# Optimization experiments

Measured on AMD Instinct MI355X. Metric: run time of the kernel, lower is better.

Reference implementation:

```python
import jax, jax.numpy as jnp
import numpy as np

D_MODEL = 1024
N_HEADS = 16
HEAD_DIM = D_MODEL // N_HEADS


def setup_inputs() -> dict:
    key = jax.random.key(0)
    ks = jax.random.split(key, 5)
    x = jax.random.normal(ks[0], (4, 2048, D_MODEL), dtype=jnp.float32)
    s = 1.0 / np.sqrt(D_MODEL)
    W_qkv = jax.random.uniform(ks[1], (D_MODEL, 3 * D_MODEL), minval=-s, maxval=s, dtype=jnp.float32)
    b_qkv = jax.random.uniform(ks[2], (3 * D_MODEL,), minval=-s, maxval=s, dtype=jnp.float32)
    W_out = jax.random.uniform(ks[3], (D_MODEL, D_MODEL), minval=-s, maxval=s, dtype=jnp.float32)
    b_out = jax.random.uniform(ks[4], (D_MODEL,), minval=-s, maxval=s, dtype=jnp.float32)
    return {"x": x, "W_qkv": W_qkv, "b_qkv": b_qkv, "W_out": W_out, "b_out": b_out}


def reference(x, W_qkv, b_qkv, W_out, b_out):
    B, S, _ = x.shape
    qkv = x @ W_qkv + b_qkv                                   # [B,S,3*D]
    qkv = qkv.reshape(B, S, 3, N_HEADS, HEAD_DIM)
    qkv = jnp.transpose(qkv, (2, 0, 3, 1, 4))                 # [3,B,H,S,Dh]
    Q, K, V = qkv[0], qkv[1], qkv[2]
    scores = jnp.einsum('bhqd,bhkd->bhqk', Q, K) / np.sqrt(HEAD_DIM)
    attn = jax.nn.softmax(scores, axis=-1)
    out = jnp.einsum('bhqk,bhkd->bhqd', attn, V)              # [B,H,S,Dh]
    out = jnp.transpose(out, (0, 2, 1, 3)).reshape(B, S, D_MODEL)
    return out @ W_out + b_out
```

## Files before the change

### kernel.cpp

```cpp
#include <hip/hip_runtime.h>
#include <stdint.h>

typedef __attribute__((ext_vector_type(8))) short short8;
typedef __attribute__((ext_vector_type(4))) float f32x4;
typedef __attribute__((ext_vector_type(16))) float f32x16;
typedef __attribute__((ext_vector_type(4))) float float4v;
typedef __attribute__((ext_vector_type(4))) unsigned short ushort4v;
typedef __attribute__((ext_vector_type(2))) unsigned int uint2v;
typedef __attribute__((ext_vector_type(4))) unsigned int uint4v;

#define MFMA16(a,b,c) __builtin_amdgcn_mfma_f32_16x16x32_bf16((a),(b),(c),0,0,0)
#define MFMA32(a,b,c) __builtin_amdgcn_mfma_f32_32x32x16_bf16((a),(b),(c),0,0,0)

typedef const __attribute__((address_space(1))) void gld_src_t;
typedef __attribute__((address_space(3))) void gld_dst_t;
#define GLOAD_LDS16(g, l) __builtin_amdgcn_global_load_lds((gld_src_t*)(g), (gld_dst_t*)(l), 16, 0, 0)

__device__ __forceinline__ unsigned short f2bf(float f) {
  union { float f; unsigned int u; } v; v.f = f;
  unsigned int u = v.u;
  unsigned int r = (u + 0x7fffu + ((u >> 16) & 1u)) >> 16;
  return (unsigned short)r;
}

__device__ __forceinline__ unsigned cvtpk(float a, float b) {
  unsigned r;
  asm("v_cvt_pk_bf16_f32 %0, %1, %2" : "=v"(r) : "v"(a), "v"(b));
  return r;
}

__device__ __forceinline__ float fexp2(float x) {
  return __builtin_amdgcn_exp2f(x);
}

__global__ __launch_bounds__(256) void cvt_f32_bf16(const float* __restrict__ in,
                                                    unsigned short* __restrict__ out) {
  int i = blockIdx.x * 256 + threadIdx.x;
  float4v v = ((const float4v*)in)[i];
  ushort4v o;
  o[0] = f2bf(v[0]); o[1] = f2bf(v[1]); o[2] = f2bf(v[2]); o[3] = f2bf(v[3]);
  ((ushort4v*)out)[i] = o;
}

__global__ __launch_bounds__(256) void cvt_transpose(const float* __restrict__ W,
                                                     unsigned short* __restrict__ WT,
                                                     int K, int N) {
  __shared__ unsigned short lds[64][72];
  int k0 = blockIdx.x * 64, n0 = blockIdx.y * 64;
  int t = threadIdx.x, tr = t >> 4, tc = t & 15;
#pragma unroll
  for (int p = 0; p < 4; ++p) {
    int k = tr + p * 16;
    float4v v = *(const float4v*)&W[(size_t)(k0 + k) * N + n0 + tc * 4];
    lds[tc * 4 + 0][k] = f2bf(v[0]);
    lds[tc * 4 + 1][k] = f2bf(v[1]);
    lds[tc * 4 + 2][k] = f2bf(v[2]);
    lds[tc * 4 + 3][k] = f2bf(v[3]);
  }
  __syncthreads();
#pragma unroll
  for (int p = 0; p < 4; ++p) {
    int n = tr + p * 16;
    ushort4v o;
    o[0] = lds[n][tc * 4 + 0]; o[1] = lds[n][tc * 4 + 1];
    o[2] = lds[n][tc * 4 + 2]; o[3] = lds[n][tc * 4 + 3];
    *(ushort4v*)&WT[(size_t)(n0 + n) * K + k0 + tc * 4] = o;
  }
}

__device__ __forceinline__ void gemm_mainloop_128(const unsigned short* __restrict__ A,
                                                  const unsigned short* __restrict__ BT,
                                                  int K, int row0, int col0,
                                                  unsigned short* Als, unsigned short* Bls,
                                                  f32x4 acc[4][4]) {
  int t = threadIdx.x;
  int w = t >> 6, l = t & 63;
  int lo = l & 15, hi = l >> 4;
  int wr = w >> 1, wc = w & 1;
  int srcC = (l & 3) ^ ((l >> 2) & 3) ^ ((l >> 4) & 3);
  const unsigned short* Ag1 = A + (size_t)(row0 + (t >> 2)) * K + srcC * 8;
  const unsigned short* Ag2 = A + (size_t)(row0 + 64 + (t >> 2)) * K + srcC * 8;
  const unsigned short* Bg1 = BT + (size_t)(col0 + (t >> 2)) * K + srcC * 8;
  const unsigned short* Bg2 = BT + (size_t)(col0 + 64 + (t >> 2)) * K + srcC * 8;
  unsigned short* Ald1 = Als + w * 512;
  unsigned short* Ald2 = Als + 2048 + w * 512;
  unsigned short* Bld1 = Bls + w * 512;
  unsigned short* Bld2 = Bls + 2048 + w * 512;
  int fs = (lo & 3) ^ ((lo >> 2) & 3);
  int aoff[4], boff[4];
#pragma unroll
  for (int m = 0; m < 4; ++m) aoff[m] = (wr * 64 + m * 16 + lo) * 32 + ((hi ^ fs) << 3);
#pragma unroll
  for (int n = 0; n < 4; ++n) boff[n] = (wc * 64 + n * 16 + lo) * 32 + ((hi ^ fs) << 3);

  for (int k0 = 0; k0 < K; k0 += 32) {
    GLOAD_LDS16(Ag1 + k0, Ald1);
    GLOAD_LDS16(Ag2 + k0, Ald2);
    GLOAD_LDS16(Bg1 + k0, Bld1);
    GLOAD_LDS16(Bg2 + k0, Bld2);
    __syncthreads();
    short8 af[4], bf[4];
#pragma unroll
    for (int m = 0; m < 4; ++m) af[m] = *(const short8*)&Als[aoff[m]];
#pragma unroll
    for (int n = 0; n < 4; ++n) bf[n] = *(const short8*)&Bls[boff[n]];
#pragma unroll
    for (int m = 0; m < 4; ++m)
#pragma unroll
      for (int n = 0; n < 4; ++n)
        acc[m][n] = MFMA16(af[m], bf[n], acc[m][n]);
    __syncthreads();
  }
}

__global__ __launch_bounds__(256) void gemm_qkv(const unsigned short* __restrict__ xb,
                                                const unsigned short* __restrict__ WT,
                                                const float* __restrict__ bias,
                                                unsigned short* __restrict__ Q,
                                                unsigned short* __restrict__ Ko,
                                                unsigned short* __restrict__ Vt) {
  __shared__ unsigned short Als[4096], Bls[4096];
  f32x4 zero = {0.f, 0.f, 0.f, 0.f};
  f32x4 acc[4][4];
#pragma unroll
  for (int m = 0; m < 4; ++m)
#pragma unroll
    for (int n = 0; n < 4; ++n) acc[m][n] = zero;
  int row0 = blockIdx.x * 128, col0 = blockIdx.y * 128;
  gemm_mainloop_128(xb, WT, 1024, row0, col0, Als, Bls, acc);

  int t = threadIdx.x, w = t >> 6, l = t & 63, lo = l & 15, hi = l >> 4;
  int wr = w >> 1, wc = w & 1;
#pragma unroll
  for (int m = 0; m < 4; ++m) {
#pragma unroll
    for (int n = 0; n < 4; ++n) {
      int col = col0 + wc * 64 + n * 16 + lo;
      float b = bias[col];
      int which = col >> 10, hd = col & 1023, h = hd >> 6, d = hd & 63;
      int row = row0 + wr * 64 + m * 16 + hi * 4;
      int bb = row >> 11, s = row & 2047;
      if (which == 2) {
        ushort4v o;
#pragma unroll
        for (int r = 0; r < 4; ++r) o[r] = f2bf(acc[m][n][r] + b);
        *(ushort4v*)&Vt[((size_t)(bb * 16 + h) * 64 + d) * 2048 + s] = o;
      } else if (which == 0) {
        size_t base = ((size_t)(bb * 16 + h) * 2048 + s) * 64 + d;
#pragma unroll
        for (int r = 0; r < 4; ++r)
          Q[base + (size_t)r * 64] = f2bf((acc[m][n][r] + b) * 0.18033688011112042f);
      } else {
        size_t base = ((size_t)(bb * 16 + h) * 2048 + s) * 64 + d;
#pragma unroll
        for (int r = 0; r < 4; ++r)
          Ko[base + (size_t)r * 64] = f2bf(acc[m][n][r] + b);
      }
    }
  }
}

__global__ __launch_bounds__(256) void gemm_out(const unsigned short* __restrict__ attn,
                                                const unsigned short* __restrict__ WT,
                                                const float* __restrict__ bias,
                                                float* __restrict__ out) {
  __shared__ unsigned short Als[4096], Bls[4096];
  f32x4 zero = {0.f, 0.f, 0.f, 0.f};
  f32x4 acc[4][4];
#pragma unroll
  for (int m = 0; m < 4; ++m)
#pragma unroll
    for (int n = 0; n < 4; ++n) acc[m][n] = zero;
  int row0 = blockIdx.x * 128, col0 = blockIdx.y * 128;
  gemm_mainloop_128(attn, WT, 1024, row0, col0, Als, Bls, acc);

  int t = threadIdx.x, w = t >> 6, l = t & 63, lo = l & 15, hi = l >> 4;
  int wr = w >> 1, wc = w & 1;
#pragma unroll
  for (int m = 0; m < 4; ++m) {
#pragma unroll
    for (int n = 0; n < 4; ++n) {
      int col = col0 + wc * 64 + n * 16 + lo;
      float b = bias[col];
#pragma unroll
      for (int r = 0; r < 4; ++r) {
        int row = row0 + wr * 64 + m * 16 + hi * 4 + r;
        out[(size_t)row * 1024 + col] = acc[m][n][r] + b;
      }
    }
  }
}

__global__ __launch_bounds__(256, 3) void attn_fwd2(const unsigned short* __restrict__ Q,
                                                    const unsigned short* __restrict__ Kg,
                                                    const unsigned short* __restrict__ Vt,
                                                    unsigned short* __restrict__ attn_out) {
  const int S = 2048;
  __shared__ unsigned short Kls[3][4096];
  __shared__ unsigned short Vls[3][4096];

  int bid = blockIdx.x;
  int swz = (bid & 7) * 128 + (bid >> 3);
  int bh = swz >> 4, qt = swz & 15;
  int t = threadIdx.x, w = t >> 6, l = t & 63;
  int lo = l & 31, hi = l >> 5;
  int qi = qt * 128 + w * 32 + lo;
  const unsigned short* Qr = Q + ((size_t)bh * S + qi) * 64 + hi * 8;
  const char* KbB = (const char*)(Kg + (size_t)bh * S * 64);
  const char* VbB = (const char*)(Vt + (size_t)bh * 64 * S);

  short8 qf[4];
#pragma unroll
  for (int ks = 0; ks < 4; ++ks) qf[ks] = *(const short8*)(Qr + ks * 16);

  short8 onesf;
#pragma unroll
  for (int e = 0; e < 8; ++e) onesf[e] = (short)0x3F80;

  int lrow = l >> 3;
  int j0 = w * 2;
  int g0B = (((l & 7) ^ lrow ^ j0) << 4);
  int g1B = (((l & 7) ^ lrow ^ (j0 + 1)) << 4);
  size_t kg0 = (size_t)(8 * j0 + lrow) * 128 + g0B;
  size_t kg1 = (size_t)(8 * j0 + 8 + lrow) * 128 + g1B;
  size_t vg0 = (size_t)(8 * j0 + lrow) * 4096 + g0B;
  size_t vg1 = (size_t)(8 * j0 + 8 + lrow) * 4096 + g1B;

  int koff0[4], koff1[4];
#pragma unroll
  for (int ks = 0; ks < 4; ++ks) {
    int srow = (lo & 7) ^ (lo >> 3);
    koff0[ks] = lo * 64 + (((2 * ks + hi) ^ srow) << 3);
    koff1[ks] = (lo + 32) * 64 + (((2 * ks + hi) ^ srow ^ 4) << 3);
  }

#define STAGE_KV(Kd, Vd, kvoff) do {                                  \
    GLOAD_LDS16(KbB + (size_t)(kvoff) * 128 + kg0, (Kd) + j0 * 512);  \
    GLOAD_LDS16(KbB + (size_t)(kvoff) * 128 + kg1, (Kd) + (j0 + 1) * 512); \
    GLOAD_LDS16(VbB + (size_t)(kvoff) * 2 + vg0, (Vd) + j0 * 512);    \
    GLOAD_LDS16(VbB + (size_t)(kvoff) * 2 + vg1, (Vd) + (j0 + 1) * 512); \
  } while (0)

  unsigned short *Kc = &Kls[0][0], *K1 = &Kls[1][0], *K2 = &Kls[2][0];
  unsigned short *Vc = &Vls[0][0], *V1 = &Vls[1][0], *V2 = &Vls[2][0];

  STAGE_KV(Kc, Vc, 0);
  STAGE_KV(K1, V1, 64);

  const f32x16 zf = {0.f,0.f,0.f,0.f,0.f,0.f,0.f,0.f,0.f,0.f,0.f,0.f,0.f,0.f,0.f,0.f};
  f32x16 ot0 = zf, ot1 = zf;
  f32x16 lacc = zf;

  for (int it = 0; it < 32; ++it) {
    asm volatile("s_waitcnt vmcnt(4)" ::: "memory");
    __builtin_amdgcn_s_barrier();
    STAGE_KV(K2, V2, ((it + 2) & 31) * 64);

    short8 kf0[4], kf1[4];
#pragma unroll
    for (int ks = 0; ks < 4; ++ks) {
      kf0[ks] = *(const short8*)&Kc[koff0[ks]];
      kf1[ks] = *(const short8*)&Kc[koff1[ks]];
    }
    f32x16 st0 = zf, st1 = zf;
    __builtin_amdgcn_s_setprio(1);
#pragma unroll
    for (int ks = 0; ks < 4; ++ks) {
      st0 = MFMA32(kf0[ks], qf[ks], st0);
      st1 = MFMA32(kf1[ks], qf[ks], st1);
    }
    __builtin_amdgcn_s_setprio(0);
    short8 vf0[4], vf1[4];
#pragma unroll
    for (int ks = 0; ks < 4; ++ks) {
      vf0[ks] = *(const short8*)&Vc[koff0[ks]];
      vf1[ks] = *(const short8*)&Vc[koff1[ks]];
    }

    short8 pb[4];
    float p[16];
#pragma unroll
    for (int r = 0; r < 16; ++r) p[r] = fexp2(st0[r]);
    {
      unsigned x0 = cvtpk(p[0], p[1]),  x1 = cvtpk(p[2], p[3]);
      unsigned y0 = cvtpk(p[4], p[5]),  y1 = cvtpk(p[6], p[7]);
      uint2v sw0 = __builtin_amdgcn_permlane32_swap(x0, y0, false, false);
      uint2v sw1 = __builtin_amdgcn_permlane32_swap(x1, y1, false, false);
      uint4v pk; pk[0] = sw0[0]; pk[1] = sw1[0]; pk[2] = sw0[1]; pk[3] = sw1[1];
      pb[0] = __builtin_bit_cast(short8, pk);
      unsigned x2 = cvtpk(p[8], p[9]),  x3 = cvtpk(p[10], p[11]);
      unsigned y2 = cvtpk(p[12], p[13]), y3 = cvtpk(p[14], p[15]);
      uint2v sw2 = __builtin_amdgcn_permlane32_swap(x2, y2, false, false);
      uint2v sw3 = __builtin_amdgcn_permlane32_swap(x3, y3, false, false);
      uint4v pk1; pk1[0] = sw2[0]; pk1[1] = sw3[0]; pk1[2] = sw2[1]; pk1[3] = sw3[1];
      pb[1] = __builtin_bit_cast(short8, pk1);
    }
#pragma unroll
    for (int r = 0; r < 16; ++r) p[r] = fexp2(st1[r]);
    {
      unsigned x0 = cvtpk(p[0], p[1]),  x1 = cvtpk(p[2], p[3]);
      unsigned y0 = cvtpk(p[4], p[5]),  y1 = cvtpk(p[6], p[7]);
      uint2v sw0 = __builtin_amdgcn_permlane32_swap(x0, y0, false, false);
      uint2v sw1 = __builtin_amdgcn_permlane32_swap(x1, y1, false, false);
      uint4v pk; pk[0] = sw0[0]; pk[1] = sw1[0]; pk[2] = sw0[1]; pk[3] = sw1[1];
      pb[2] = __builtin_bit_cast(short8, pk);
      unsigned x2 = cvtpk(p[8], p[9]),  x3 = cvtpk(p[10], p[11]);
      unsigned y2 = cvtpk(p[12], p[13]), y3 = cvtpk(p[14], p[15]);
      uint2v sw2 = __builtin_amdgcn_permlane32_swap(x2, y2, false, false);
      uint2v sw3 = __builtin_amdgcn_permlane32_swap(x3, y3, false, false);
      uint4v pk1; pk1[0] = sw2[0]; pk1[1] = sw3[0]; pk1[2] = sw2[1]; pk1[3] = sw3[1];
      pb[3] = __builtin_bit_cast(short8, pk1);
    }

    __builtin_amdgcn_s_setprio(1);
#pragma unroll
    for (int ks = 0; ks < 4; ++ks) {
      ot0 = MFMA32(vf0[ks], pb[ks], ot0);
      ot1 = MFMA32(vf1[ks], pb[ks], ot1);
      lacc = MFMA32(onesf, pb[ks], lacc);
    }
    __builtin_amdgcn_s_setprio(0);

    unsigned short* tk = Kc; Kc = K1; K1 = K2; K2 = tk;
    unsigned short* tv = Vc; Vc = V1; V1 = V2; V2 = tv;
  }

  float inv = 1.0f / lacc[0];
  int b = bh >> 4, h = bh & 15;
  unsigned short* orow = attn_out + ((size_t)(b * 2048 + qi)) * 1024 + h * 64 + 4 * hi;
#pragma unroll
  for (int g = 0; g < 4; ++g) {
    uint2v u0, u1;
    u0[0] = cvtpk(ot0[4*g + 0] * inv, ot0[4*g + 1] * inv);
    u0[1] = cvtpk(ot0[4*g + 2] * inv, ot0[4*g + 3] * inv);
    u1[0] = cvtpk(ot1[4*g + 0] * inv, ot1[4*g + 1] * inv);
    u1[1] = cvtpk(ot1[4*g + 2] * inv, ot1[4*g + 3] * inv);
    *(uint2v*)(orow + 8 * g) = u0;
    *(uint2v*)(orow + 32 + 8 * g) = u1;
  }
}

extern "C" void kernel_launch(void* const* d_in, const int* in_sizes, int n_in,
                              void* d_out, int out_size, void* d_ws, size_t ws_size,
                              hipStream_t stream) {
  (void)in_sizes; (void)n_in; (void)out_size; (void)ws_size;
  const float* x     = (const float*)d_in[0];
  const float* W_qkv = (const float*)d_in[1];
  const float* b_qkv = (const float*)d_in[2];
  const float* W_out = (const float*)d_in[3];
  const float* b_out = (const float*)d_in[4];
  float* out = (float*)d_out;
  char* ws = (char*)d_ws;
  unsigned short* xb    = (unsigned short*)(ws);
  unsigned short* WqkvT = (unsigned short*)(ws + 16777216);
  unsigned short* WoutT = (unsigned short*)(ws + 23068672);
  unsigned short* Qb    = (unsigned short*)(ws + 25165824);
  unsigned short* Kb    = (unsigned short*)(ws + 41943040);
  unsigned short* Vtb   = (unsigned short*)(ws + 75497472);
  unsigned short* attnb = (unsigned short*)(ws + 92274688);

  cvt_f32_bf16<<<8192, 256, 0, stream>>>(x, xb);
  cvt_transpose<<<dim3(16, 48), 256, 0, stream>>>(W_qkv, WqkvT, 1024, 3072);
  cvt_transpose<<<dim3(16, 16), 256, 0, stream>>>(W_out, WoutT, 1024, 1024);
  gemm_qkv<<<dim3(64, 24), 256, 0, stream>>>(xb, WqkvT, b_qkv, Qb, Kb, Vtb);
  attn_fwd2<<<1024, 256, 0, stream>>>(Qb, Kb, Vtb, attnb);
  gemm_out<<<dim3(64, 8), 256, 0, stream>>>(attnb, WoutT, b_out, out);
}
```

Measured before the change: 198.2 us.

## Triple-buffer LDS in GEMM mainloop to overlap global loads with MFMA

Switches the shared GEMM mainloop from a single LDS buffer with two barriers per k-step to a three-stage ring. Loads are prefetched two stages ahead, with a vmcnt wait and a single barrier per iteration. This is meant to hide global-to-LDS latency behind the MFMA work in both the QKV and output projections. It triples LDS use per block, which may lower occupancy, and it issues redundant wrap-around prefetches at the tail.

```diff
diff --git a/kernel.cpp b/kernel.cpp
--- a/kernel.cpp
+++ b/kernel.cpp
@@ -71,7 +71,8 @@
 __device__ __forceinline__ void gemm_mainloop_128(const unsigned short* __restrict__ A,
                                                   const unsigned short* __restrict__ BT,
                                                   int K, int row0, int col0,
-                                                  unsigned short* Als, unsigned short* Bls,
+                                                  unsigned short (*Als)[4096],
+                                                  unsigned short (*Bls)[4096],
                                                   f32x4 acc[4][4]) {
   int t = threadIdx.x;
   int w = t >> 6, l = t & 63;
@@ -82,10 +83,7 @@
   const unsigned short* Ag2 = A + (size_t)(row0 + 64 + (t >> 2)) * K + srcC * 8;
   const unsigned short* Bg1 = BT + (size_t)(col0 + (t >> 2)) * K + srcC * 8;
   const unsigned short* Bg2 = BT + (size_t)(col0 + 64 + (t >> 2)) * K + srcC * 8;
-  unsigned short* Ald1 = Als + w * 512;
-  unsigned short* Ald2 = Als + 2048 + w * 512;
-  unsigned short* Bld1 = Bls + w * 512;
-  unsigned short* Bld2 = Bls + 2048 + w * 512;
+  int d1 = w * 512, d2 = 2048 + w * 512;
   int fs = (lo & 3) ^ ((lo >> 2) & 3);
   int aoff[4], boff[4];
 #pragma unroll
@@ -93,24 +91,39 @@
 #pragma unroll
   for (int n = 0; n < 4; ++n) boff[n] = (wc * 64 + n * 16 + lo) * 32 + ((hi ^ fs) << 3);
 
-  for (int k0 = 0; k0 < K; k0 += 32) {
-    GLOAD_LDS16(Ag1 + k0, Ald1);
-    GLOAD_LDS16(Ag2 + k0, Ald2);
-    GLOAD_LDS16(Bg1 + k0, Bld1);
-    GLOAD_LDS16(Bg2 + k0, Bld2);
-    __syncthreads();
+#define GSTAGE(Ad, Bd, k0) do {              \
+    GLOAD_LDS16(Ag1 + (k0), (Ad) + d1);      \
+    GLOAD_LDS16(Ag2 + (k0), (Ad) + d2);      \
+    GLOAD_LDS16(Bg1 + (k0), (Bd) + d1);      \
+    GLOAD_LDS16(Bg2 + (k0), (Bd) + d2);      \
+  } while (0)
+
+  unsigned short *A0 = &Als[0][0], *A1 = &Als[1][0], *A2 = &Als[2][0];
+  unsigned short *B0 = &Bls[0][0], *B1 = &Bls[1][0], *B2 = &Bls[2][0];
+  int nk = K >> 5;
+  GSTAGE(A0, B0, 0);
+  GSTAGE(A1, B1, 32);
+  for (int k = 0; k < nk; ++k) {
+    asm volatile("s_waitcnt vmcnt(4)" ::: "memory");
+    __builtin_amdgcn_s_barrier();
+    __builtin_amdgcn_sched_barrier(0);
+    int kn = ((k + 2) & (nk - 1)) * 32;
+    GSTAGE(A2, B2, kn);
     short8 af[4], bf[4];
 #pragma unroll
-    for (int m = 0; m < 4; ++m) af[m] = *(const short8*)&Als[aoff[m]];
-#pragma unroll
-    for (int n = 0; n < 4; ++n) bf[n] = *(const short8*)&Bls[boff[n]];
+    for (int m = 0; m < 4; ++m) af[m] = *(const short8*)&A0[aoff[m]];
+#pragma unroll
+    for (int n = 0; n < 4; ++n) bf[n] = *(const short8*)&B0[boff[n]];
 #pragma unroll
     for (int m = 0; m < 4; ++m)
 #pragma unroll
       for (int n = 0; n < 4; ++n)
         acc[m][n] = MFMA16(af[m], bf[n], acc[m][n]);
-    __syncthreads();
-  }
+    __builtin_amdgcn_sched_barrier(0);
+    unsigned short* ta = A0; A0 = A1; A1 = A2; A2 = ta;
+    unsigned short* tb = B0; B0 = B1; B1 = B2; B2 = tb;
+  }
+#undef GSTAGE
 }
 
 __global__ __launch_bounds__(256) void gemm_qkv(const unsigned short* __restrict__ xb,
@@ -119,7 +132,7 @@
                                                 unsigned short* __restrict__ Q,
                                                 unsigned short* __restrict__ Ko,
                                                 unsigned short* __restrict__ Vt) {
-  __shared__ unsigned short Als[4096], Bls[4096];
+  __shared__ unsigned short Als[3][4096], Bls[3][4096];
   f32x4 zero = {0.f, 0.f, 0.f, 0.f};
   f32x4 acc[4][4];
 #pragma unroll
@@ -164,7 +177,7 @@
                                                 const unsigned short* __restrict__ WT,
                                                 const float* __restrict__ bias,
                                                 float* __restrict__ out) {
-  __shared__ unsigned short Als[4096], Bls[4096];
+  __shared__ unsigned short Als[3][4096], Bls[3][4096];
   f32x4 zero = {0.f, 0.f, 0.f, 0.f};
   f32x4 acc[4][4];
 #pragma unroll
```

Result: slower. 203.5 us (+2.7%).
